# Optimization experiments

Measured on AMD Instinct MI355X. Metric: run time of the kernel, lower is better.

The kernel has to match this reference:

```python
import jax, jax.numpy as jnp
import numpy as np
import math

D_MODEL = 1024
N_HEADS = 16
D_HEAD = D_MODEL // N_HEADS
B, L = 4, 2048


def setup_inputs() -> dict:
    key = jax.random.key(0)
    ks = jax.random.split(key, 9)
    s = 1.0 / math.sqrt(D_MODEL)
    x = jax.random.normal(ks[0], (B, L, D_MODEL), dtype=jnp.float32)
    # causal mask, broadcastable over batch and heads
    attn_mask = jnp.tril(jnp.ones((L, L), dtype=jnp.int32))[None, None, :, :]
    Wq = jax.random.uniform(ks[1], (D_MODEL, D_MODEL), jnp.float32, -s, s)
    bq = jax.random.uniform(ks[2], (D_MODEL,), jnp.float32, -s, s)
    Wk = jax.random.uniform(ks[3], (D_MODEL, D_MODEL), jnp.float32, -s, s)
    bk = jax.random.uniform(ks[4], (D_MODEL,), jnp.float32, -s, s)
    Wv = jax.random.uniform(ks[5], (D_MODEL, D_MODEL), jnp.float32, -s, s)
    bv = jax.random.uniform(ks[6], (D_MODEL,), jnp.float32, -s, s)
    Wo = jax.random.uniform(ks[7], (D_MODEL, D_MODEL), jnp.float32, -s, s)
    bo = jax.random.uniform(ks[8], (D_MODEL,), jnp.float32, -s, s)
    return {"x": x, "attn_mask": attn_mask, "Wq": Wq, "bq": bq, "Wk": Wk,
            "bk": bk, "Wv": Wv, "bv": bv, "Wo": Wo, "bo": bo}


def reference(x, attn_mask, Wq, bq, Wk, bk, Wv, bv, Wo, bo):
    Bn, Ln, Dn = x.shape
    scale = 1.0 / math.sqrt(D_HEAD)

    def split_heads(t):  # [B,L,D] -> [B,H,L,dh]
        return t.reshape(Bn, Ln, N_HEADS, D_HEAD).transpose(0, 2, 1, 3)

    q = split_heads(x @ Wq + bq)
    k = split_heads(x @ Wk + bk)
    v = split_heads(x @ Wv + bv)
    scores = jnp.einsum('bhqd,bhkd->bhqk', q, k) * scale
    scores = jnp.where(attn_mask == 0, jnp.float32(-jnp.inf), scores)
    attn = jax.nn.softmax(scores, axis=-1)  # dropout p=0.0 -> identity
    ctx = jnp.einsum('bhqk,bhkd->bhqd', attn, v)
    ctx = ctx.transpose(0, 2, 1, 3).reshape(Bn, Ln, Dn)
    return ctx @ Wo + bo
```

## Files before the change

kernel.cpp:

```cpp
#include <hip/hip_runtime.h>


typedef unsigned short u16;
typedef __attribute__((ext_vector_type(8))) short short8;
typedef __attribute__((ext_vector_type(4))) float floatx4;
typedef __attribute__((ext_vector_type(2))) unsigned int uint2v;

#define NEG_BIG (-1e30f)
#define SCL_LOG2E 0.1803368801111244f

__device__ __forceinline__ u16 f2bf(float f) {
  unsigned int u = __builtin_bit_cast(unsigned int, f);
  u += 0x7fffu + ((u >> 16) & 1u);
  return (u16)(u >> 16);
}

__device__ __forceinline__ short8 cvt8(const float* __restrict__ p) {
  const floatx4 a = *(const floatx4*)p;
  const floatx4 b = *(const floatx4*)(p + 4);
  short8 r;
  r[0] = (short)f2bf(a[0]); r[1] = (short)f2bf(a[1]);
  r[2] = (short)f2bf(a[2]); r[3] = (short)f2bf(a[3]);
  r[4] = (short)f2bf(b[0]); r[5] = (short)f2bf(b[1]);
  r[6] = (short)f2bf(b[2]); r[7] = (short)f2bf(b[3]);
  return r;
}

__device__ __forceinline__ void gll16(const u16* g, u16* l) {
  __builtin_amdgcn_global_load_lds((const __attribute__((address_space(1))) void*)g,
                                   (__attribute__((address_space(3))) void*)l,
                                   16, 0, 0);
}

__global__ void cvt_x(const float* __restrict__ x, u16* __restrict__ xb) {
  const int i = blockIdx.x * 256 + threadIdx.x;
  *(short8*)(xb + (size_t)i * 8) = cvt8(x + (size_t)i * 8);
}

__global__ void transpose4(const float* __restrict__ s0, const float* __restrict__ s1,
                           const float* __restrict__ s2, const float* __restrict__ s3,
                           u16* __restrict__ d0, u16* __restrict__ d1,
                           u16* __restrict__ d2, u16* __restrict__ d3) {
  __shared__ u16 tile[64][72];
  const float* src; u16* dst;
  switch (blockIdx.z) {
    case 0: src = s0; dst = d0; break;
    case 1: src = s1; dst = d1; break;
    case 2: src = s2; dst = d2; break;
    default: src = s3; dst = d3; break;
  }
  const int t = threadIdx.x;
  const int c = t & 63, rg = t >> 6;
  const int x0 = blockIdx.x * 64, y0 = blockIdx.y * 64;
#pragma unroll
  for (int i = 0; i < 16; ++i) {
    const int row = rg * 16 + i;
    tile[row][c] = f2bf(src[(size_t)(y0 + row) * 1024 + x0 + c]);
  }
  __syncthreads();
#pragma unroll
  for (int i = 0; i < 16; ++i) {
    const int row = rg * 16 + i;
    dst[(size_t)(x0 + row) * 1024 + y0 + c] = tile[c][row];
  }
}

__global__ void transpose_v(const u16* __restrict__ Vb, u16* __restrict__ Vt) {
  __shared__ u16 tile[64][66];
  const int bh = blockIdx.y;
  const int l0 = blockIdx.x * 64;
  const size_t base = (size_t)bh * (2048 * 64);
  const int t = threadIdx.x;
#pragma unroll
  for (int c = t; c < 512; c += 256) {
    const int row = c >> 3, cc = c & 7;
    *(short8*)&tile[row][cc * 8] =
        *(const short8*)(Vb + base + (size_t)(l0 + row) * 64 + cc * 8);
  }
  __syncthreads();
  const int c2 = t & 63, rg = t >> 6;
#pragma unroll
  for (int i = 0; i < 16; ++i) {
    const int dr = rg * 16 + i;
    Vt[base + (size_t)dr * 2048 + l0 + c2] = tile[c2][dr];
  }
}

__global__ __launch_bounds__(256, 2) void gemm_qkv(
    const u16* __restrict__ A, const u16* __restrict__ Bt,
    const float* __restrict__ bq, const float* __restrict__ bk,
    const float* __restrict__ bv,
    u16* __restrict__ Qb, u16* __restrict__ Kb, u16* __restrict__ Vb) {
  const int K = 1024;
  __shared__ __align__(16) u16 As[128 * 32];
  __shared__ __align__(16) u16 Bs[128 * 32];
  const int t = threadIdx.x;
  const int w = t >> 6, l = t & 63;
  const int quad = l >> 4, l16 = l & 15;
  const int m0 = blockIdx.y * 128, n0 = blockIdx.x * 128;
  const int wr = w >> 1, wc = w & 1;

  floatx4 acc[4][4] = {};

  for (int k0 = 0; k0 < K; k0 += 32) {
    __syncthreads();
#pragma unroll
    for (int p = 0; p < 2; ++p) {
      const int c0 = (p * 4 + w) * 64;
      const int c = c0 + l;
      const int row = c >> 2;
      const int koff = (c & 3) * 8;
      gll16(A + (size_t)(m0 + row) * K + k0 + koff, &As[c0 * 8]);
      gll16(Bt + (size_t)(n0 + row) * K + k0 + koff, &Bs[c0 * 8]);
    }
    __syncthreads();

    short8 af[4], bf[4];
#pragma unroll
    for (int i = 0; i < 4; ++i)
      af[i] = *(const short8*)&As[(wr * 64 + i * 16 + l16) * 32 + quad * 8];
#pragma unroll
    for (int j = 0; j < 4; ++j)
      bf[j] = *(const short8*)&Bs[(wc * 64 + j * 16 + l16) * 32 + quad * 8];
#pragma unroll
    for (int i = 0; i < 4; ++i)
#pragma unroll
      for (int j = 0; j < 4; ++j)
        acc[i][j] = __builtin_amdgcn_mfma_f32_16x16x32_bf16(af[i], bf[j], acc[i][j], 0, 0, 0);
  }

  const int seg = n0 >> 10;
  const float* bias = (seg == 0) ? bq : (seg == 1) ? bk : bv;
  u16* dst = (seg == 0) ? Qb : (seg == 1) ? Kb : Vb;
  const float scl = (seg == 0) ? SCL_LOG2E : 1.0f;
#pragma unroll
  for (int j = 0; j < 4; ++j) {
    const int nn = (n0 & 1023) + wc * 64 + j * 16 + l16;
    const float bvs = bias[nn];
    const int h = nn >> 6, dh = nn & 63;
#pragma unroll
    for (int i = 0; i < 4; ++i) {
      const int rb = m0 + wr * 64 + i * 16 + quad * 4;
#pragma unroll
      for (int r = 0; r < 4; ++r) {
        const int m = rb + r;
        const int b = m >> 11, ll = m & 2047;
        dst[((size_t)(b * 16 + h) * 2048 + ll) * 64 + dh] = f2bf((acc[i][j][r] + bvs) * scl);
      }
    }
  }
}

__global__ __launch_bounds__(256, 2) void gemm_out(
    const u16* __restrict__ A, const u16* __restrict__ Bt,
    const float* __restrict__ bias, float* __restrict__ C, int M, int N, int K) {
  __shared__ __align__(16) u16 As[128 * 32];
  __shared__ __align__(16) u16 Bs[128 * 32];
  const int t = threadIdx.x;
  const int w = t >> 6, l = t & 63;
  const int quad = l >> 4, l16 = l & 15;
  const int m0 = blockIdx.y * 128, n0 = blockIdx.x * 128;
  const int wr = w >> 1, wc = w & 1;

  floatx4 acc[4][4] = {};

  for (int k0 = 0; k0 < K; k0 += 32) {
    __syncthreads();
#pragma unroll
    for (int p = 0; p < 2; ++p) {
      const int c0 = (p * 4 + w) * 64;
      const int c = c0 + l;
      const int row = c >> 2;
      const int koff = (c & 3) * 8;
      gll16(A + (size_t)(m0 + row) * K + k0 + koff, &As[c0 * 8]);
      gll16(Bt + (size_t)(n0 + row) * K + k0 + koff, &Bs[c0 * 8]);
    }
    __syncthreads();

    short8 af[4], bf[4];
#pragma unroll
    for (int i = 0; i < 4; ++i)
      af[i] = *(const short8*)&As[(wr * 64 + i * 16 + l16) * 32 + quad * 8];
#pragma unroll
    for (int j = 0; j < 4; ++j)
      bf[j] = *(const short8*)&Bs[(wc * 64 + j * 16 + l16) * 32 + quad * 8];
#pragma unroll
    for (int i = 0; i < 4; ++i)
#pragma unroll
      for (int j = 0; j < 4; ++j)
        acc[i][j] = __builtin_amdgcn_mfma_f32_16x16x32_bf16(af[i], bf[j], acc[i][j], 0, 0, 0);
  }

#pragma unroll
  for (int j = 0; j < 4; ++j) {
    const int n = n0 + wc * 64 + j * 16 + l16;
    const float bvs = bias[n];
#pragma unroll
    for (int i = 0; i < 4; ++i) {
      const int rb = m0 + wr * 64 + i * 16 + quad * 4;
#pragma unroll
      for (int r = 0; r < 4; ++r)
        C[(size_t)(rb + r) * N + n] = acc[i][j][r] + bvs;
    }
  }
}

__global__ __launch_bounds__(512, 4) void attn_kernel(
    const u16* __restrict__ Q, const u16* __restrict__ K,
    const u16* __restrict__ Vt, u16* __restrict__ ctx) {
  __shared__ __align__(16) u16 Ks[2][64 * 64];
  __shared__ __align__(16) u16 Vs[2][64 * 64];
  __shared__ __align__(16) u16 Ps[8 * 16 * 64];

  const int t = threadIdx.x;
  const int w = t >> 6, l = t & 63;
  const int quad = l >> 4, l16 = l & 15;
  const int lin = blockIdx.y * 8 + blockIdx.x;
  const int bh = (lin & 7) * 8 + ((lin >> 3) & 7);
  const int pp = lin >> 6;
  const size_t base = (size_t)bh * (2048 * 64);
  const int b = bh >> 4, h = bh & 15;
  u16* Pw = &Ps[w * 16 * 64];
  unsigned int* Pw32 = (unsigned int*)Pw;

  const int pc = w * 64 + l;
  const int sr = pc >> 3, sc = (pc & 7) ^ (sr & 7);
  const int swz = (l16 & 7);

  auto run_seg = [&](int p) {
    const int q0 = p * 128;
    const int nkt = 2 * p + 2;
    const int qg = q0 + w * 16 + l16;
    const int qmax = q0 + w * 16 + 15;
    const int qmin = q0 + w * 16;

    short8 aq[2];
#pragma unroll
    for (int ks = 0; ks < 2; ++ks)
      aq[ks] = *(const short8*)(Q + base + (size_t)qg * 64 + ks * 32 + quad * 8);

    gll16(K + base + (size_t)sr * 64 + sc * 8, &Ks[0][(w * 64) * 8]);
    gll16(Vt + base + (size_t)sr * 2048 + sc * 8, &Vs[0][(w * 64) * 8]);

    floatx4 o[4] = {};
    float mrun = NEG_BIG, lsum = 0.f;

    for (int kt = 0; kt < nkt; ++kt) {
      const int cur = kt & 1, nxt = cur ^ 1;
      __syncthreads();
      if (kt + 1 < nkt) {
        const int kn = (kt + 1) * 64;
        gll16(K + base + (size_t)(kn + sr) * 64 + sc * 8, &Ks[nxt][(w * 64) * 8]);
        gll16(Vt + base + (size_t)sr * 2048 + kn + sc * 8, &Vs[nxt][(w * 64) * 8]);
      }
      const int kbase = kt * 64;
      if (kbase > qmax) continue;
      const bool masked = (kbase + 63 > qmin);

      floatx4 s[4] = {};
      __builtin_amdgcn_s_setprio(1);
#pragma unroll
      for (int ks = 0; ks < 2; ++ks)
#pragma unroll
        for (int tn = 0; tn < 4; ++tn) {
          const short8 bk = *(const short8*)&Ks[cur][(tn * 16 + l16) * 64 + (((ks * 4 + quad) ^ swz) << 3)];
          s[tn] = __builtin_amdgcn_mfma_f32_16x16x32_bf16(bk, aq[ks], s[tn], 0, 0, 0);
        }
      __builtin_amdgcn_s_setprio(0);

      float mx = NEG_BIG;
      if (masked) {
#pragma unroll
        for (int tn = 0; tn < 4; ++tn)
#pragma unroll
          for (int r = 0; r < 4; ++r) {
            float v = s[tn][r];
            if (kbase + tn * 16 + quad * 4 + r > qg) v = NEG_BIG;
            s[tn][r] = v;
            mx = fmaxf(mx, v);
          }
      } else {
#pragma unroll
        for (int tn = 0; tn < 4; ++tn)
#pragma unroll
          for (int r = 0; r < 4; ++r) mx = fmaxf(mx, s[tn][r]);
      }
      mx = fmaxf(mx, __shfl_xor(mx, 16));
      mx = fmaxf(mx, __shfl_xor(mx, 32));

      if (!__all(mx - mrun <= 8.f)) {
        const float mnew = fmaxf(mrun, mx);
        const float al = exp2f(mrun - mnew);
        mrun = mnew;
        lsum *= al;
#pragma unroll
        for (int td = 0; td < 4; ++td)
#pragma unroll
          for (int r = 0; r < 4; ++r) o[td][r] *= al;
      }

      float rs = 0.f;
#pragma unroll
      for (int tn = 0; tn < 4; ++tn)
#pragma unroll
        for (int r = 0; r < 4; ++r) {
          const float pv = exp2f(s[tn][r] - mrun);
          s[tn][r] = pv;
          rs += pv;
        }

#pragma unroll
      for (int tn = 0; tn < 4; ++tn) {
        unsigned int p0, p1;
        asm("v_cvt_pk_bf16_f32 %0, %1, %2"
            : "=v"(p0) : "v"(s[tn][0]), "v"(s[tn][1]));
        asm("v_cvt_pk_bf16_f32 %0, %1, %2"
            : "=v"(p1) : "v"(s[tn][2]), "v"(s[tn][3]));
        const int cc = (2 * tn + (quad >> 1)) ^ swz;
        uint2v pr; pr.x = p0; pr.y = p1;
        *(uint2v*)&Pw32[l16 * 32 + cc * 4 + 2 * (quad & 1)] = pr;
      }
      rs += __shfl_xor(rs, 16);
      rs += __shfl_xor(rs, 32);
      lsum += rs;
      __asm__ volatile("s_waitcnt lgkmcnt(0)" ::: "memory");
      __builtin_amdgcn_wave_barrier();

      short8 ap[2];
#pragma unroll
      for (int ks = 0; ks < 2; ++ks)
        ap[ks] = *(const short8*)&Pw[l16 * 64 + (((ks * 4 + quad) ^ swz) << 3)];

      __builtin_amdgcn_s_setprio(1);
#pragma unroll
      for (int ks = 0; ks < 2; ++ks)
#pragma unroll
        for (int td = 0; td < 4; ++td) {
          const short8 bv = *(const short8*)&Vs[cur][(td * 16 + l16) * 64 + (((ks * 4 + quad) ^ swz) << 3)];
          o[td] = __builtin_amdgcn_mfma_f32_16x16x32_bf16(bv, ap[ks], o[td], 0, 0, 0);
        }
      __builtin_amdgcn_s_setprio(0);
    }

    const float inv = 1.f / lsum;
    u16* crow = ctx + ((size_t)(b * 2048 + qg)) * 1024 + h * 64;
#pragma unroll
    for (int td = 0; td < 4; ++td) {
      unsigned int lo, hi;
      asm("v_cvt_pk_bf16_f32 %0, %1, %2"
          : "=v"(lo) : "v"(o[td][0] * inv), "v"(o[td][1] * inv));
      asm("v_cvt_pk_bf16_f32 %0, %1, %2"
          : "=v"(hi) : "v"(o[td][2] * inv), "v"(o[td][3] * inv));
      uint2v pk;
      pk.x = lo; pk.y = hi;
      *(uint2v*)(crow + td * 16 + quad * 4) = pk;
    }
  };

  run_seg(15 - pp);
  __syncthreads();
  run_seg(pp);
}

extern "C" void kernel_launch(void* const* d_in, const int* in_sizes, int n_in,
                              void* d_out, int out_size, void* d_ws, size_t ws_size,
                              hipStream_t stream) {
  const float* x  = (const float*)d_in[0];
  const float* Wq = (const float*)d_in[2];
  const float* bq = (const float*)d_in[3];
  const float* Wk = (const float*)d_in[4];
  const float* bk = (const float*)d_in[5];
  const float* Wv = (const float*)d_in[6];
  const float* bv = (const float*)d_in[7];
  const float* Wo = (const float*)d_in[8];
  const float* bo = (const float*)d_in[9];

  u16* ws = (u16*)d_ws;
  const size_t WSZ = 1u << 20;
  const size_t TSZ = 8u << 20;
  u16* WqT = ws;
  u16* WkT = ws + WSZ;
  u16* WvT = ws + 2 * WSZ;
  u16* WoT = ws + 3 * WSZ;
  u16* xb  = ws + 4 * WSZ;
  u16* Qb  = xb + TSZ;
  u16* Kb  = Qb + TSZ;
  u16* Vb  = Kb + TSZ;
  u16* Vtb = xb;
  u16* Ctx = Vb;

  const dim3 tb(256);
  cvt_x<<<dim3(4096), tb, 0, stream>>>(x, xb);
  transpose4<<<dim3(16, 16, 4), tb, 0, stream>>>(Wq, Wk, Wv, Wo, WqT, WkT, WvT, WoT);
  gemm_qkv<<<dim3(24, 64), tb, 0, stream>>>(xb, WqT, bq, bk, bv, Qb, Kb, Vb);
  transpose_v<<<dim3(32, 64), tb, 0, stream>>>(Vb, Vtb);
  attn_kernel<<<dim3(8, 64), dim3(512), 0, stream>>>(Qb, Kb, Vtb, Ctx);
  gemm_out<<<dim3(8, 64), tb, 0, stream>>>(Ctx, WoT, bo, (float*)d_out, 8192, 1024, 1024);
}
```

Baseline: 292.3 us.

## Compute softmax row sums via MFMA, use max3, and remap GEMM block order

```diff
diff --git a/kernel.cpp b/kernel.cpp
--- a/kernel.cpp
+++ b/kernel.cpp
@@ -13,6 +13,12 @@
   unsigned int u = __builtin_bit_cast(unsigned int, f);
   u += 0x7fffu + ((u >> 16) & 1u);
   return (u16)(u >> 16);
+}
+
+__device__ __forceinline__ float max3f(float a, float b, float c) {
+  float d;
+  asm("v_max3_f32 %0, %1, %2, %3" : "=v"(d) : "v"(a), "v"(b), "v"(c));
+  return d;
 }
 
 __device__ __forceinline__ short8 cvt8(const float* __restrict__ p) {
@@ -97,7 +103,9 @@
   const int t = threadIdx.x;
   const int w = t >> 6, l = t & 63;
   const int quad = l >> 4, l16 = l & 15;
-  const int m0 = blockIdx.y * 128, n0 = blockIdx.x * 128;
+  const int lin = blockIdx.y * 24 + blockIdx.x;
+  const int nl = (lin & 7) * 192 + (lin >> 3);
+  const int m0 = (nl / 24) * 128, n0 = (nl % 24) * 128;
   const int wr = w >> 1, wc = w & 1;
 
   floatx4 acc[4][4] = {};
@@ -159,7 +167,9 @@
   const int t = threadIdx.x;
   const int w = t >> 6, l = t & 63;
   const int quad = l >> 4, l16 = l & 15;
-  const int m0 = blockIdx.y * 128, n0 = blockIdx.x * 128;
+  const int lin = blockIdx.y * 8 + blockIdx.x;
+  const int nl = (lin & 7) * 64 + (lin >> 3);
+  const int m0 = (nl >> 3) * 128, n0 = (nl & 7) * 128;
   const int wr = w >> 1, wc = w & 1;
 
   floatx4 acc[4][4] = {};
@@ -223,6 +233,9 @@
   u16* Pw = &Ps[w * 16 * 64];
   unsigned int* Pw32 = (unsigned int*)Pw;
 
+  const short8 vone = {(short)0x3F80, (short)0x3F80, (short)0x3F80, (short)0x3F80,
+                       (short)0x3F80, (short)0x3F80, (short)0x3F80, (short)0x3F80};
+
   const int pc = w * 64 + l;
   const int sr = pc >> 3, sc = (pc & 7) ^ (sr & 7);
   const int swz = (l16 & 7);
@@ -243,7 +256,8 @@
     gll16(Vt + base + (size_t)sr * 2048 + sc * 8, &Vs[0][(w * 64) * 8]);
 
     floatx4 o[4] = {};
-    float mrun = NEG_BIG, lsum = 0.f;
+    floatx4 lacc = {};
+    float mrun = NEG_BIG;
 
     for (int kt = 0; kt < nkt; ++kt) {
       const int cur = kt & 1, nxt = cur ^ 1;
@@ -268,23 +282,19 @@
         }
       __builtin_amdgcn_s_setprio(0);
 
-      float mx = NEG_BIG;
       if (masked) {
 #pragma unroll
         for (int tn = 0; tn < 4; ++tn)
 #pragma unroll
-          for (int r = 0; r < 4; ++r) {
-            float v = s[tn][r];
-            if (kbase + tn * 16 + quad * 4 + r > qg) v = NEG_BIG;
-            s[tn][r] = v;
-            mx = fmaxf(mx, v);
-          }
-      } else {
-#pragma unroll
-        for (int tn = 0; tn < 4; ++tn)
-#pragma unroll
-          for (int r = 0; r < 4; ++r) mx = fmaxf(mx, s[tn][r]);
+          for (int r = 0; r < 4; ++r)
+            if (kbase + tn * 16 + quad * 4 + r > qg) s[tn][r] = NEG_BIG;
       }
+      const float m0t = max3f(s[0][0], s[0][1], s[0][2]);
+      const float m1t = max3f(s[0][3], s[1][0], s[1][1]);
+      const float m2t = max3f(s[1][2], s[1][3], s[2][0]);
+      const float m3t = max3f(s[2][1], s[2][2], s[2][3]);
+      const float m4t = max3f(s[3][0], s[3][1], s[3][2]);
+      float mx = fmaxf(max3f(m0t, m1t, m2t), max3f(m3t, m4t, s[3][3]));
       mx = fmaxf(mx, __shfl_xor(mx, 16));
       mx = fmaxf(mx, __shfl_xor(mx, 32));
 
@@ -292,22 +302,19 @@
         const float mnew = fmaxf(mrun, mx);
         const float al = exp2f(mrun - mnew);
         mrun = mnew;
-        lsum *= al;
+#pragma unroll
+        for (int r = 0; r < 4; ++r) lacc[r] *= al;
 #pragma unroll
         for (int td = 0; td < 4; ++td)
 #pragma unroll
           for (int r = 0; r < 4; ++r) o[td][r] *= al;
       }
 
-      float rs = 0.f;
 #pragma unroll
       for (int tn = 0; tn < 4; ++tn)
 #pragma unroll
-        for (int r = 0; r < 4; ++r) {
-          const float pv = exp2f(s[tn][r] - mrun);
-          s[tn][r] = pv;
-          rs += pv;
-        }
+        for (int r = 0; r < 4; ++r)
+          s[tn][r] = exp2f(s[tn][r] - mrun);
 
 #pragma unroll
       for (int tn = 0; tn < 4; ++tn) {
@@ -320,9 +327,6 @@
         uint2v pr; pr.x = p0; pr.y = p1;
         *(uint2v*)&Pw32[l16 * 32 + cc * 4 + 2 * (quad & 1)] = pr;
       }
-      rs += __shfl_xor(rs, 16);
-      rs += __shfl_xor(rs, 32);
-      lsum += rs;
       __asm__ volatile("s_waitcnt lgkmcnt(0)" ::: "memory");
       __builtin_amdgcn_wave_barrier();
 
@@ -332,6 +336,8 @@
         ap[ks] = *(const short8*)&Pw[l16 * 64 + (((ks * 4 + quad) ^ swz) << 3)];
 
       __builtin_amdgcn_s_setprio(1);
+      lacc = __builtin_amdgcn_mfma_f32_16x16x32_bf16(vone, ap[0], lacc, 0, 0, 0);
+      lacc = __builtin_amdgcn_mfma_f32_16x16x32_bf16(vone, ap[1], lacc, 0, 0, 0);
 #pragma unroll
       for (int ks = 0; ks < 2; ++ks)
 #pragma unroll
@@ -342,7 +348,7 @@
       __builtin_amdgcn_s_setprio(0);
     }
 
-    const float inv = 1.f / lsum;
+    const float inv = 1.f / lacc[0];
     u16* crow = ctx + ((size_t)(b * 2048 + qg)) * 1024 + h * 64;
 #pragma unroll
     for (int td = 0; td < 4; ++td) {
```

Result: faster. 285.8 us (-2.2%).
